# Optimization experiments

Hardware: AMD Instinct MI355X
Metric: run time of the kernel (lower is better)

The kernel has to match this reference:

```python
import jax, jax.numpy as jnp
import numpy as np
from jax import lax

EPS = 1e-5
B, CIN, H, W = 4, 512, 64, 64
CI = CIN // 4          # inter_channels = 128
CQK = CI // 8          # PAM query/key channels = 16
NC = 19                # num_classes


def conv2d(x, w, pad):
    return lax.conv_general_dilated(x, w, (1, 1), [(pad, pad), (pad, pad)],
                                    dimension_numbers=('NCHW', 'OIHW', 'NCHW'))


def bn_relu(x, g, b, m, v):
    # eval-mode BatchNorm2d followed by ReLU
    inv = g * lax.rsqrt(v + EPS)
    return jax.nn.relu(x * inv[None, :, None, None] + (b - m * inv)[None, :, None, None])


def setup_inputs() -> dict:
    key = jax.random.key(0)
    ks = iter(jax.random.split(key, 40))
    rn = lambda shape, s=0.02: (jax.random.normal(next(ks), shape, dtype=jnp.float32) * s)
    ones = lambda n: jnp.ones((n,), jnp.float32)
    zeros = lambda n: jnp.zeros((n,), jnp.float32)
    inp = {
        'x': jax.random.normal(next(ks), (B, CIN, H, W), dtype=jnp.float32),
        # conv_p1: 3x3 conv (no bias) + BN
        'wp1': rn((CI, CIN, 3, 3)),
        'bnp1_w': ones(CI), 'bnp1_b': zeros(CI), 'bnp1_m': zeros(CI), 'bnp1_v': ones(CI),
        # PAM 1x1 convs
        'qw': rn((CQK, CI, 1, 1)), 'qb': zeros(CQK),
        'kw': rn((CQK, CI, 1, 1)), 'kb': zeros(CQK),
        'vw': rn((CI, CI, 1, 1)), 'vb': zeros(CI),
        'pam_gamma': jnp.full((1,), 0.5, jnp.float32),
        # conv_p2
        'wp2': rn((CI, CI, 3, 3)),
        'bnp2_w': ones(CI), 'bnp2_b': zeros(CI), 'bnp2_m': zeros(CI), 'bnp2_v': ones(CI),
        # conv_c1
        'wc1': rn((CI, CIN, 3, 3)),
        'bnc1_w': ones(CI), 'bnc1_b': zeros(CI), 'bnc1_m': zeros(CI), 'bnc1_v': ones(CI),
        'cam_gamma': jnp.full((1,), 0.5, jnp.float32),
        # conv_c2
        'wc2': rn((CI, CI, 3, 3)),
        'bnc2_w': ones(CI), 'bnc2_b': zeros(CI), 'bnc2_m': zeros(CI), 'bnc2_v': ones(CI),
        # classifier heads (dropout is eval-mode identity)
        'cls_w': rn((NC, CI, 1, 1)), 'cls_b': zeros(NC),
        'auxp_w': rn((NC, CI, 1, 1)), 'auxp_b': zeros(NC),
        'auxc_w': rn((NC, CI, 1, 1)), 'auxc_b': zeros(NC),
    }
    return inp


def pam(x, qw, qb, kw, kb, vw, vb, gamma):
    b, c, h, w = x.shape
    n = h * w
    q = (conv2d(x, qw, 0) + qb[None, :, None, None]).reshape(b, -1, n)  # [B,CQK,N]
    k = (conv2d(x, kw, 0) + kb[None, :, None, None]).reshape(b, -1, n)  # [B,CQK,N]
    v = (conv2d(x, vw, 0) + vb[None, :, None, None]).reshape(b, c, n)   # [B,C,N]
    attn = jax.nn.softmax(jnp.einsum('bcn,bcm->bnm', q, k), axis=-1)    # [B,N,N]
    out = jnp.einsum('bcm,bnm->bcn', v, attn).reshape(b, c, h, w)
    return gamma * out + x


def cam(x, gamma):
    b, c, h, w = x.shape
    f = x.reshape(b, c, -1)                                             # [B,C,N]
    attn = jax.nn.softmax(jnp.einsum('bin,bjn->bij', f, f), axis=-1)    # [B,C,C]
    out = jnp.einsum('bij,bjn->bin', attn, f).reshape(b, c, h, w)
    return gamma * out + x


def _forward(x, wp1, bnp1_w, bnp1_b, bnp1_m, bnp1_v,
             qw, qb, kw, kb, vw, vb, pam_gamma,
             wp2, bnp2_w, bnp2_b, bnp2_m, bnp2_v,
             wc1, bnc1_w, bnc1_b, bnc1_m, bnc1_v, cam_gamma,
             wc2, bnc2_w, bnc2_b, bnc2_m, bnc2_v,
             cls_w, cls_b, auxp_w, auxp_b, auxc_w, auxc_b):
    feat_p = bn_relu(conv2d(x, wp1, 1), bnp1_w, bnp1_b, bnp1_m, bnp1_v)
    feat_p = pam(feat_p, qw, qb, kw, kb, vw, vb, pam_gamma)
    feat_p = bn_relu(conv2d(feat_p, wp2, 1), bnp2_w, bnp2_b, bnp2_m, bnp2_v)

    feat_c = bn_relu(conv2d(x, wc1, 1), bnc1_w, bnc1_b, bnc1_m, bnc1_v)
    feat_c = cam(feat_c, cam_gamma)
    feat_c = bn_relu(conv2d(feat_c, wc2, 1), bnc2_w, bnc2_b, bnc2_m, bnc2_v)

    feat = feat_p + feat_c
    out = conv2d(feat, cls_w, 0) + cls_b[None, :, None, None]
    out_p = conv2d(feat_p, auxp_w, 0) + auxp_b[None, :, None, None]
    out_c = conv2d(feat_c, auxc_w, 0) + auxc_b[None, :, None, None]
    return out, out_p, out_c


def reference(x, wp1, bnp1_w, bnp1_b, bnp1_m, bnp1_v,
              qw, qb, kw, kb, vw, vb, pam_gamma,
              wp2, bnp2_w, bnp2_b, bnp2_m, bnp2_v,
              wc1, bnc1_w, bnc1_b, bnc1_m, bnc1_v, cam_gamma,
              wc2, bnc2_w, bnc2_b, bnc2_m, bnc2_v,
              cls_w, cls_b, auxp_w, auxp_b, auxc_w, auxc_b):
    return _forward(x, wp1, bnp1_w, bnp1_b, bnp1_m, bnp1_v,
                    qw, qb, kw, kb, vw, vb, pam_gamma,
                    wp2, bnp2_w, bnp2_b, bnp2_m, bnp2_v,
                    wc1, bnc1_w, bnc1_b, bnc1_m, bnc1_v, cam_gamma,
                    wc2, bnc2_w, bnc2_b, bnc2_m, bnc2_v,
                    cls_w, cls_b, auxp_w, auxp_b, auxc_w, auxc_b)
```

## Files before the change

### kernel.cpp

```cpp
#include <hip/hip_runtime.h>
#include <cstdint>
#include <cstddef>


using s16x8 = __attribute__((ext_vector_type(8))) short;
using u16x8 = __attribute__((ext_vector_type(8))) unsigned short;
using u16x4 = __attribute__((ext_vector_type(4))) unsigned short;
using f32x4 = __attribute__((ext_vector_type(4))) float;
using f32x16 = __attribute__((ext_vector_type(16))) float;
using u32x4v = __attribute__((ext_vector_type(4))) unsigned;

__device__ __forceinline__ f32x4 mfma16(u16x8 a, u16x8 b, f32x4 c) {
  return __builtin_amdgcn_mfma_f32_16x16x32_bf16(
      __builtin_bit_cast(s16x8, a), __builtin_bit_cast(s16x8, b), c, 0, 0, 0);
}
__device__ __forceinline__ f32x16 mfma32(u16x8 a, u16x8 b, f32x16 c) {
  return __builtin_amdgcn_mfma_f32_32x32x16_bf16(
      __builtin_bit_cast(s16x8, a), __builtin_bit_cast(s16x8, b), c, 0, 0, 0);
}
__device__ __forceinline__ float bf2f(unsigned short u) {
  return __builtin_bit_cast(float, (unsigned)u << 16);
}
__device__ __forceinline__ unsigned short f2bf(float f) {
  unsigned u = __builtin_bit_cast(unsigned, f);
  u += 0x7fffu + ((u >> 16) & 1u);
  return (unsigned short)(u >> 16);
}
__device__ __forceinline__ unsigned cvt_pk_bf16(float lo, float hi) {
  unsigned r;
  asm("v_cvt_pk_bf16_f32 %0, %1, %2" : "=v"(r) : "v"(lo), "v"(hi));
  return r;
}
__device__ __forceinline__ u16x8 ld8(const unsigned short* p) {
  return *reinterpret_cast<const u16x8*>(p);
}
__device__ __forceinline__ void gload16(const void* g, void* l) {
  __builtin_amdgcn_global_load_lds(
      (const __attribute__((address_space(1))) void*)g,
      (__attribute__((address_space(3))) void*)l, 16, 0, 0);
}

#define OFF_XT    ((size_t)0)
#define OFF_FP1   ((size_t)19464192)
#define OFF_FC1   ((size_t)24330240)
#define ZERO_BYTES ((size_t)29196288)
#define OFF_FP0   ((size_t)29196288)
#define OFF_FC0   ((size_t)33390592)
#define OFF_FP2   ((size_t)37584896)
#define OFF_FC2   ((size_t)41779200)
#define OFF_WT1   ((size_t)45973504)
#define OFF_WT2   ((size_t)48332800)
#define OFF_QKW   ((size_t)48922624)
#define OFF_VWW   ((size_t)48930816)
#define OFF_HWW   ((size_t)48963584)
#define OFF_BNSS  ((size_t)48988160)
#define OFF_ATTN  ((size_t)48992256)
#define OFF_Q     OFF_FP2
#define OFF_K     (OFF_FP2 + 524288)
#define OFF_V     OFF_FC2

__global__ __launch_bounds__(256) void k_xpose(const float* __restrict__ x,
                                               unsigned short* __restrict__ xt) {
  __shared__ float tile[128][65];
  const int t = threadIdx.x;
  const int blk = blockIdx.x;
  const int cb = blk & 3;
  const int h = (blk >> 2) & 63;
  const int b = blk >> 8;
  const float* src = x + ((size_t)(b * 512 + cb * 128) * 64 + h) * 64;
  const int w = t & 63, cr = t >> 6;
  for (int i = 0; i < 32; ++i) tile[cr + i * 4][w] = src[(size_t)(cr + i * 4) * 4096 + w];
  __syncthreads();
  const int w2 = t >> 2, cg = t & 3;
  const int cic = cb * 2 + (cg >> 1);
  const int kk = ((w2 + 1) & 7) << 3;
  unsigned short* dst =
      xt + (((size_t)(b * 8 + cic) * 66 + h + 1) * 72 + (w2 + 1)) * 64 + (cg & 1) * 32;
#pragma unroll
  for (int j = 0; j < 32; j += 4) {
    const int sb = (cg >> 1) * 64 + (((cg & 1) * 32 + j) ^ kk);
    u16x4 pk;
    pk[0] = f2bf(tile[sb + 0][w2]);
    pk[1] = f2bf(tile[sb + 1][w2]);
    pk[2] = f2bf(tile[sb + 2][w2]);
    pk[3] = f2bf(tile[sb + 3][w2]);
    *reinterpret_cast<u16x4*>(dst + j) = pk;
  }
}

struct PackArgs {
  const float *wp1, *wc1, *wp2, *wc2, *qw, *kw, *vw, *clsw, *apw, *acw;
  const float *g1p, *b1p, *m1p, *v1p, *g1c, *b1c, *m1c, *v1c;
  const float *g2p, *b2p, *m2p, *v2p, *g2c, *b2c, *m2c, *v2c;
  unsigned short *wt1, *wt2, *qkw, *vww, *hww;
  float* bnss;
};
__global__ __launch_bounds__(256) void k_pack(PackArgs A) {
  const int i = blockIdx.x * 256 + threadIdx.x;
  const int N1 = 2 * 8 * 9 * 128 * 64;
  const int N2 = N1 + 2 * 2 * 9 * 128 * 64;
  const int N3 = N2 + 2 * 16 * 128;
  const int N4 = N3 + 128 * 128;
  const int N5 = N4 + 3 * 32 * 128;
  const int N6 = N5 + 8 * 128;
  if (i < N1) {
    int ci = i & 63, co = (i >> 6) & 127;
    int rest = i >> 13;
    int tap = rest % 9, cc = rest / 9;
    int cic = cc & 7, brr = cc >> 3;
    const float* s = brr ? A.wc1 : A.wp1;
    int cis = ci ^ ((co & 7) << 3);
    A.wt1[i] = f2bf(s[(size_t)(co * 512 + cic * 64 + cis) * 9 + tap]);
  } else if (i < N2) {
    int k = i - N1;
    int ci = k & 63, co = (k >> 6) & 127;
    int rest = k >> 13;
    int tap = rest % 9, cc = rest / 9;
    int cic = cc & 1, brr = cc >> 1;
    const float* s = brr ? A.wc2 : A.wp2;
    int cis = ci ^ ((co & 7) << 3);
    A.wt2[k] = f2bf(s[(size_t)(co * 128 + cic * 64 + cis) * 9 + tap]);
  } else if (i < N3) {
    int k = i - N2;
    int ci = k & 127, q = k >> 7;
    const float* s = (q < 16) ? A.qw : A.kw;
    A.qkw[k] = f2bf(s[(q & 15) * 128 + ci]);
  } else if (i < N4) {
    int k = i - N3;
    A.vww[k] = f2bf(A.vw[k]);
  } else if (i < N5) {
    int k = i - N4;
    int ci = k & 127, co = (k >> 7) & 31, hd = k >> 12;
    const float* s = hd == 0 ? A.clsw : (hd == 1 ? A.apw : A.acw);
    A.hww[k] = (co < 19) ? f2bf(s[co * 128 + ci]) : (unsigned short)0;
  } else if (i < N6) {
    int k = i - N5;
    int j = k & 127, seg = k >> 7;
    const float *g, *bb, *mm, *vv;
    switch (seg >> 1) {
      case 0: g = A.g1p; bb = A.b1p; mm = A.m1p; vv = A.v1p; break;
      case 1: g = A.g1c; bb = A.b1c; mm = A.m1c; vv = A.v1c; break;
      case 2: g = A.g2p; bb = A.b2p; mm = A.m2p; vv = A.v2p; break;
      default: g = A.g2c; bb = A.b2c; mm = A.m2c; vv = A.v2c; break;
    }
    float sc = g[j] * rsqrtf(vv[j] + 1e-5f);
    A.bnss[k] = (seg & 1) ? (bb[j] - mm[j] * sc) : sc;
  }
}

template <int NCHUNK>
__global__ __launch_bounds__(256, 1) void k_conv3x3(
    const unsigned short* __restrict__ in0, const unsigned short* __restrict__ in1,
    const unsigned short* __restrict__ wt, const float* __restrict__ bnb,
    unsigned short* __restrict__ out0, unsigned short* __restrict__ out1) {
  __shared__ unsigned short Awin[4 * 72 * 64];
  __shared__ unsigned short Wbuf[2][3 * 128 * 64];
  const int bid = blockIdx.x;
  const int ht = bid & 31;
  const int b = (bid >> 5) & 3;
  const int br = bid >> 7;
  const unsigned short* inp = br ? in1 : in0;
  const unsigned short* wbr = wt + (size_t)br * NCHUNK * 9 * 128 * 64;
  const float* scale = bnb + br * 256;
  const float* shiftp = scale + 128;
  unsigned short* outp = br ? out1 : out0;
  const int tid = threadIdx.x;
  const int lane = tid & 63, wv = tid >> 6;
  const int l31 = lane & 31, hi = lane >> 5;
  const int hi16 = hi * 16;
  const int nq = wv & 1, ch = wv >> 1;
  const int wn = nq * 64, cob = ch * 64;
  const int h0 = ht * 2;

  int aw[2], arow[2];
#pragma unroll
  for (int mf = 0; mf < 2; ++mf) {
    int n = wn + mf * 32 + l31;
    aw[mf] = n & 63;
    arow[mf] = (n >> 6) * 72;
  }
  int bvbase[2];
#pragma unroll
  for (int nf = 0; nf < 2; ++nf) bvbase[nf] = (cob + nf * 32 + l31) * 128;
  const int bkey = (l31 & 7) << 4;

  f32x16 acc[2][2];
#pragma unroll
  for (int mf = 0; mf < 2; ++mf)
#pragma unroll
    for (int nf = 0; nf < 2; ++nf) acc[mf][nf] = (f32x16)0.f;

  u16x8 streg[9];
  auto sloadA = [&](int c) {
    const char* sr =
        (const char*)(inp + (((size_t)(b * NCHUNK + c) * 66 + h0) * 72) * 64);
#pragma unroll
    for (int i = 0; i < 9; ++i)
      streg[i] = *(const u16x8*)(sr + i * 4096 + tid * 16);
  };
  auto swriteA = [&]() {
    char* dp = (char*)Awin;
#pragma unroll
    for (int i = 0; i < 9; ++i)
      *(u16x8*)(dp + i * 4096 + tid * 16) = streg[i];
  };
  auto stageW = [&](int bi, int T) {
    const char* src = (const char*)wbr + (size_t)T * 49152;
    char* dst = (char*)&Wbuf[bi][0];
#pragma unroll
    for (int i = 0; i < 12; ++i)
      gload16(src + i * 4096 + tid * 16, dst + i * 4096 + tid * 16);
  };

  auto compute = [&](int g, int bi) {
    const char* ab = (const char*)Awin;
    const char* wb = (const char*)&Wbuf[bi][0];
#pragma unroll
    for (int tl = 0; tl < 3; ++tl) {
      int abase[2], akey[2];
#pragma unroll
      for (int mf = 0; mf < 2; ++mf) {
        int wc = aw[mf] + tl;
        abase[mf] = ((arow[mf] + g * 72 + wc) << 7);
        akey[mf] = (wc & 7) << 4;
      }
      const int wtl = tl << 14;
#pragma unroll
      for (int s = 0; s < 4; ++s) {
        const int ko = s * 32 + hi16;
        u16x8 av[2], bv[2];
#pragma unroll
        for (int mf = 0; mf < 2; ++mf)
          av[mf] = *(const u16x8*)(ab + abase[mf] + (ko ^ akey[mf]));
#pragma unroll
        for (int nf = 0; nf < 2; ++nf)
          bv[nf] = *(const u16x8*)(wb + wtl + bvbase[nf] + (ko ^ bkey));
#pragma unroll
        for (int mf = 0; mf < 2; ++mf)
#pragma unroll
          for (int nf = 0; nf < 2; ++nf)
            acc[mf][nf] = mfma32(av[mf], bv[nf], acc[mf][nf]);
      }
    }
  };

  const int total = 3 * NCHUNK;
  sloadA(0);
  stageW(0, 0);
  swriteA();
  stageW(1, 1);
  asm volatile("s_waitcnt vmcnt(12) lgkmcnt(0)\ns_barrier" ::: "memory");
  if (NCHUNK > 1) sloadA(1);

#pragma unroll 1
  for (int c = 0; c < NCHUNK; ++c) {
#pragma unroll
    for (int g = 0; g < 3; ++g) {
      const int T = c * 3 + g;
      compute(g, T & 1);
      if (T + 1 < total) {
        asm volatile("s_waitcnt lgkmcnt(0)\ns_barrier" ::: "memory");
        bool issuedA = false;
        if (g == 2) {
          swriteA();
          if (c + 2 < NCHUNK) {
            sloadA(c + 2);
            issuedA = true;
          }
        }
        if (T + 2 < total) {
          stageW((T + 2) & 1, T + 2);
          if (issuedA)
            asm volatile("s_waitcnt vmcnt(21) lgkmcnt(0)\ns_barrier" ::: "memory");
          else
            asm volatile("s_waitcnt vmcnt(12) lgkmcnt(0)\ns_barrier" ::: "memory");
        } else {
          asm volatile("s_waitcnt vmcnt(0) lgkmcnt(0)\ns_barrier" ::: "memory");
        }
      }
    }
  }

#pragma unroll
  for (int nf = 0; nf < 2; ++nf) {
    const int co = cob + nf * 32 + l31;
    const float sc = scale[co], sh = shiftp[co];
#pragma unroll
    for (int mf = 0; mf < 2; ++mf)
#pragma unroll
      for (int r = 0; r < 16; ++r) {
        int n = wn + mf * 32 + (r & 3) + 8 * (r >> 2) + 4 * hi;
        float y = acc[mf][nf][r] * sc + sh;
        y = y > 0.f ? y : 0.f;
        outp[((size_t)b * 4096 + (size_t)(h0 + (n >> 6)) * 64 + (n & 63)) * 128 + co] =
            f2bf(y);
      }
  }
}

__global__ __launch_bounds__(256) void k_qkv(
    const unsigned short* __restrict__ fp0, const unsigned short* __restrict__ qkw,
    const unsigned short* __restrict__ vww, const float* __restrict__ qb,
    const float* __restrict__ kb, const float* __restrict__ vb,
    unsigned short* __restrict__ Q, unsigned short* __restrict__ K,
    unsigned short* __restrict__ V2) {
  const int bid = blockIdx.x;
  const int nt = bid & 63, b = bid >> 6;
  const int lane = threadIdx.x & 63, wv = threadIdx.x >> 6;
  const int lg = lane >> 4, l15 = lane & 15;
  const int n = nt * 64 + wv * 16 + l15;
  const unsigned short* fbase = fp0 + ((size_t)b * 4096 + n) * 128 + lg * 8;
  f32x4 vacc[8];
#pragma unroll
  for (int mf = 0; mf < 8; ++mf) vacc[mf] = (f32x4){0.f, 0.f, 0.f, 0.f};
  f32x4 qacc = {0.f, 0.f, 0.f, 0.f}, kacc = {0.f, 0.f, 0.f, 0.f};
#pragma unroll
  for (int kc = 0; kc < 128; kc += 32) {
    u16x8 fb = ld8(fbase + kc);
    u16x8 qa = ld8(qkw + (size_t)l15 * 128 + lg * 8 + kc);
    u16x8 ka = ld8(qkw + 2048 + (size_t)l15 * 128 + lg * 8 + kc);
    qacc = mfma16(qa, fb, qacc);
    kacc = mfma16(ka, fb, kacc);
#pragma unroll
    for (int mf = 0; mf < 8; ++mf) {
      u16x8 va = ld8(vww + (size_t)(mf * 16 + l15) * 128 + lg * 8 + kc);
      vacc[mf] = mfma16(va, fb, vacc[mf]);
    }
  }
  const float LOG2E = 1.44269504088896f;
#pragma unroll
  for (int r = 0; r < 4; ++r) {
    int cq = lg * 4 + r;
    Q[(size_t)(b * 4096 + n) * 16 + cq] = f2bf((qacc[r] + qb[cq]) * LOG2E);
    K[(size_t)(b * 4096 + n) * 16 + cq] = f2bf(kacc[r] + kb[cq]);
  }
#pragma unroll
  for (int mf = 0; mf < 8; ++mf)
#pragma unroll
    for (int r = 0; r < 4; ++r) {
      int c = mf * 16 + lg * 4 + r;
      V2[((size_t)(b * 512 + (n >> 3)) * 128 + c) * 8 + (n & 7)] =
          f2bf(vacc[mf][r] + vb[c]);
    }
}

__global__ __launch_bounds__(512, 1) void k_pam(
    const unsigned short* __restrict__ Q, const unsigned short* __restrict__ K,
    const unsigned short* __restrict__ V2, const unsigned short* __restrict__ fp0,
    unsigned short* __restrict__ fp1, const float* __restrict__ pg) {
  __shared__ float obuf[2][3][16][64][4];
  __shared__ float lred[8][64];
  const int bid = blockIdx.x;
  const int qt = bid & 63, b = bid >> 6;
  const int tid = threadIdx.x;
  const int lane = tid & 63, wv = tid >> 6;
  const int qsub = wv >> 2, mq = wv & 3;
  const int l31 = lane & 31, hi = lane >> 5;
  const int q0 = qt * 64 + qsub * 32;
  const unsigned short* Qp = Q + (size_t)b * 65536;
  const unsigned short* Kp = K + (size_t)b * 65536;
  const unsigned short* Vp = V2 + (size_t)b * 524288;
  const int hi8 = hi * 8;

  const u16x8 qB = ld8(Qp + (size_t)(q0 + l31) * 16 + hi8);

  f32x16 oacc[4];
#pragma unroll
  for (int ch = 0; ch < 4; ++ch) oacc[ch] = (f32x16)0.f;
  float dsum = 0.f;

  auto loadK = [&](int t) -> u16x8 {
    return ld8(Kp + (size_t)(t * 32 + l31) * 16 + hi8);
  };
  auto loadV = [&](int t, u16x8 (&vf)[8]) {
#pragma unroll
    for (int kc = 0; kc < 2; ++kc)
#pragma unroll
      for (int ch = 0; ch < 4; ++ch)
        vf[kc * 4 + ch] =
            ld8(Vp + (size_t)(t * 4 + kc * 2 + hi) * 1024 + (ch * 32 + l31) * 8);
  };
  auto body = [&](u16x8 kA, u16x8 (&vf)[8]) {
    f32x16 pacc = mfma32(kA, qB, (f32x16)0.f);
    float p[16];
#pragma unroll
    for (int r = 0; r < 16; ++r) p[r] = exp2f(pacc[r]);
    dsum += (((p[0] + p[1]) + (p[2] + p[3])) + ((p[4] + p[5]) + (p[6] + p[7]))) +
            (((p[8] + p[9]) + (p[10] + p[11])) + ((p[12] + p[13]) + (p[14] + p[15])));
    unsigned X[8], S[8];
#pragma unroll
    for (int j = 0; j < 8; ++j) X[j] = cvt_pk_bf16(p[2 * j], p[2 * j + 1]);
#pragma unroll
    for (int j = 0; j < 8; ++j) S[j] = __shfl_xor(X[j], 32, 64);
    const bool hc = hi != 0;
    u32x4v w0, w1;
    w0[0] = hc ? S[2] : X[0];
    w0[1] = hc ? S[3] : X[1];
    w0[2] = hc ? X[2] : S[0];
    w0[3] = hc ? X[3] : S[1];
    w1[0] = hc ? S[6] : X[4];
    w1[1] = hc ? S[7] : X[5];
    w1[2] = hc ? X[6] : S[4];
    w1[3] = hc ? X[7] : S[5];
    u16x8 f0 = __builtin_bit_cast(u16x8, w0);
    u16x8 f1 = __builtin_bit_cast(u16x8, w1);
#pragma unroll
    for (int ch = 0; ch < 4; ++ch) oacc[ch] = mfma32(f0, vf[ch], oacc[ch]);
#pragma unroll
    for (int ch = 0; ch < 4; ++ch) oacc[ch] = mfma32(f1, vf[4 + ch], oacc[ch]);
  };

  const int t0 = mq * 32;
  u16x8 kA0 = loadK(t0), kA1;
  u16x8 vf0[8], vf1[8];
  loadV(t0, vf0);
#pragma unroll 1
  for (int t = 0; t < 32; t += 2) {
    kA1 = loadK(t0 + t + 1);
    loadV(t0 + t + 1, vf1);
    body(kA0, vf0);
    if (t + 2 < 32) {
      kA0 = loadK(t0 + t + 2);
      loadV(t0 + t + 2, vf0);
    }
    body(kA1, vf1);
  }

  dsum += __shfl_xor(dsum, 32, 64);
  lred[wv][lane] = dsum;
  if (mq) {
#pragma unroll
    for (int ch = 0; ch < 4; ++ch)
#pragma unroll
      for (int j = 0; j < 4; ++j) {
        f32x4 v = {oacc[ch][4 * j + 0], oacc[ch][4 * j + 1], oacc[ch][4 * j + 2],
                   oacc[ch][4 * j + 3]};
        *reinterpret_cast<f32x4*>(&obuf[qsub][mq - 1][ch * 4 + j][lane][0]) = v;
      }
  }
  __syncthreads();
  if (mq == 0) {
    const float dtot = lred[qsub * 4 + 0][lane] + lred[qsub * 4 + 1][lane] +
                       lred[qsub * 4 + 2][lane] + lred[qsub * 4 + 3][lane];
#pragma unroll
    for (int ch = 0; ch < 4; ++ch)
#pragma unroll
      for (int j = 0; j < 4; ++j) {
        f32x4 s0 = *reinterpret_cast<const f32x4*>(&obuf[qsub][0][ch * 4 + j][lane][0]);
        f32x4 s1 = *reinterpret_cast<const f32x4*>(&obuf[qsub][1][ch * 4 + j][lane][0]);
        f32x4 s2 = *reinterpret_cast<const f32x4*>(&obuf[qsub][2][ch * 4 + j][lane][0]);
#pragma unroll
        for (int r = 0; r < 4; ++r)
          oacc[ch][4 * j + r] += (s0[r] + s1[r]) + s2[r];
      }
    const float rden = 1.f / dtot;
    const float gm = pg[0];
    float rdr[16];
#pragma unroll
    for (int r = 0; r < 16; ++r)
      rdr[r] = __shfl(rden, (r & 3) + 8 * (r >> 2) + 4 * hi, 64);
#pragma unroll
    for (int ch = 0; ch < 4; ++ch) {
      const int c = ch * 32 + l31;
#pragma unroll
      for (int r = 0; r < 16; ++r) {
        const int n = q0 + (r & 3) + 8 * (r >> 2) + 4 * hi;
        const int wp = (n & 63) + 1;
        float o = gm * oacc[ch][r] * rdr[r] +
                  bf2f(fp0[((size_t)b * 4096 + n) * 128 + c]);
        fp1[(((size_t)(b * 2 + (c >> 6)) * 66 + (n >> 6) + 1) * 72 + wp) * 64 +
            ((c & 63) ^ ((wp & 7) << 3))] = f2bf(o);
      }
    }
  }
}

__global__ __launch_bounds__(256) void k_gram(const unsigned short* __restrict__ fc0,
                                              float* __restrict__ Gp) {
  __shared__ float fl[32][132];
  const int bid = blockIdx.x;
  const int nc = bid & 63, b = bid >> 6;
  const int t = threadIdx.x;
  const int i = t >> 1, jh = (t & 1) * 64;
  float acc[64];
#pragma unroll
  for (int j = 0; j < 64; ++j) acc[j] = 0.f;
  for (int c2 = 0; c2 < 2; ++c2) {
    const int n0 = nc * 64 + c2 * 32;
    {
      int nn = t >> 3, kh = t & 7;
      const unsigned short* src = fc0 + ((size_t)b * 4096 + n0 + nn) * 128 + kh * 16;
      u16x8 v0 = ld8(src), v1 = ld8(src + 8);
#pragma unroll
      for (int e = 0; e < 8; ++e) {
        fl[nn][kh * 16 + e] = bf2f(v0[e]);
        fl[nn][kh * 16 + 8 + e] = bf2f(v1[e]);
      }
    }
    __syncthreads();
    for (int nn = 0; nn < 32; ++nn) {
      float fi = fl[nn][i];
      const float4* row = reinterpret_cast<const float4*>(&fl[nn][jh]);
#pragma unroll
      for (int j4 = 0; j4 < 16; ++j4) {
        float4 fv = row[j4];
        acc[4 * j4 + 0] += fi * fv.x;
        acc[4 * j4 + 1] += fi * fv.y;
        acc[4 * j4 + 2] += fi * fv.z;
        acc[4 * j4 + 3] += fi * fv.w;
      }
    }
    __syncthreads();
  }
  float* dst = Gp + (((size_t)b * 64 + nc) * 128 + i) * 128 + jh;
  float4* dst4 = reinterpret_cast<float4*>(dst);
#pragma unroll
  for (int j4 = 0; j4 < 16; ++j4)
    dst4[j4] = make_float4(acc[4 * j4], acc[4 * j4 + 1], acc[4 * j4 + 2], acc[4 * j4 + 3]);
}

__global__ __launch_bounds__(128) void k_softm(const float* __restrict__ Gp,
                                               unsigned short* __restrict__ attn) {
  const int bid = blockIdx.x;
  const int i = bid & 127, b = bid >> 7;
  const int j = threadIdx.x;
  float g = 0.f;
  for (int nc = 0; nc < 64; ++nc) g += Gp[(((size_t)b * 64 + nc) * 128 + i) * 128 + j];
  __shared__ float red[2], red2[2];
  float m = g;
  m = fmaxf(m, __shfl_xor(m, 1, 64));
  m = fmaxf(m, __shfl_xor(m, 2, 64));
  m = fmaxf(m, __shfl_xor(m, 4, 64));
  m = fmaxf(m, __shfl_xor(m, 8, 64));
  m = fmaxf(m, __shfl_xor(m, 16, 64));
  m = fmaxf(m, __shfl_xor(m, 32, 64));
  const int wvi = j >> 6;
  if ((j & 63) == 0) red[wvi] = m;
  __syncthreads();
  m = fmaxf(red[0], red[1]);
  float e = __expf(g - m);
  float s = e;
  s += __shfl_xor(s, 1, 64);
  s += __shfl_xor(s, 2, 64);
  s += __shfl_xor(s, 4, 64);
  s += __shfl_xor(s, 8, 64);
  s += __shfl_xor(s, 16, 64);
  s += __shfl_xor(s, 32, 64);
  if ((j & 63) == 0) red2[wvi] = s;
  __syncthreads();
  s = red2[0] + red2[1];
  attn[((size_t)b * 128 + i) * 128 + j] = f2bf(e / s);
}

__global__ __launch_bounds__(256) void k_camout(
    const unsigned short* __restrict__ fc0, const unsigned short* __restrict__ attn,
    const float* __restrict__ cg, unsigned short* __restrict__ fc1) {
  const int bid = blockIdx.x;
  const int nt = bid & 63, b = bid >> 6;
  const int lane = threadIdx.x & 63, wv = threadIdx.x >> 6;
  const int lg = lane >> 4, l15 = lane & 15;
  const int n = nt * 64 + wv * 16 + l15;
  const unsigned short* fbase = fc0 + ((size_t)b * 4096 + n) * 128 + lg * 8;
  const unsigned short* abase = attn + (size_t)b * 16384 + lg * 8;
  f32x4 acc[8];
#pragma unroll
  for (int mf = 0; mf < 8; ++mf) acc[mf] = (f32x4){0.f, 0.f, 0.f, 0.f};
#pragma unroll
  for (int kc = 0; kc < 128; kc += 32) {
    u16x8 fb = ld8(fbase + kc);
#pragma unroll
    for (int mf = 0; mf < 8; ++mf) {
      u16x8 aa = ld8(abase + (size_t)(mf * 16 + l15) * 128 + kc);
      acc[mf] = mfma16(aa, fb, acc[mf]);
    }
  }
  const float gm = cg[0];
  const int nn = nt * 64 + wv * 16 + l15;
  const int wp = (nn & 63) + 1;
#pragma unroll
  for (int mf = 0; mf < 8; ++mf)
#pragma unroll
    for (int r = 0; r < 4; ++r) {
      int c = mf * 16 + lg * 4 + r;
      float o = gm * acc[mf][r] + bf2f(fc0[((size_t)b * 4096 + nn) * 128 + c]);
      fc1[(((size_t)(b * 2 + (c >> 6)) * 66 + (nn >> 6) + 1) * 72 + wp) * 64 +
          ((c & 63) ^ ((wp & 7) << 3))] = f2bf(o);
    }
}

__global__ __launch_bounds__(256) void k_heads(
    const unsigned short* __restrict__ fp2, const unsigned short* __restrict__ fc2,
    const unsigned short* __restrict__ hw, const float* __restrict__ clsb,
    const float* __restrict__ apb, const float* __restrict__ acb,
    float* __restrict__ out) {
  const int bid = blockIdx.x;
  const int nt = bid & 63, b = bid >> 6;
  const int lane = threadIdx.x & 63, wv = threadIdx.x >> 6;
  const int lg = lane >> 4, l15 = lane & 15;
  const int n = nt * 64 + wv * 16 + l15;
  const unsigned short* pb = fp2 + (size_t)(b * 4096 + n) * 128 + lg * 8;
  const unsigned short* cb = fc2 + (size_t)(b * 4096 + n) * 128 + lg * 8;
  f32x4 acc[3][2];
#pragma unroll
  for (int hd = 0; hd < 3; ++hd)
#pragma unroll
    for (int mf = 0; mf < 2; ++mf) acc[hd][mf] = (f32x4){0.f, 0.f, 0.f, 0.f};
#pragma unroll
  for (int kc = 0; kc < 128; kc += 32) {
    u16x8 vp = ld8(pb + kc);
    u16x8 vc = ld8(cb + kc);
    u16x8 vs;
#pragma unroll
    for (int e = 0; e < 8; ++e) vs[e] = f2bf(bf2f(vp[e]) + bf2f(vc[e]));
#pragma unroll
    for (int mf = 0; mf < 2; ++mf) {
      u16x8 a0 = ld8(hw + (size_t)(0 * 32 + mf * 16 + l15) * 128 + lg * 8 + kc);
      u16x8 a1 = ld8(hw + (size_t)(1 * 32 + mf * 16 + l15) * 128 + lg * 8 + kc);
      u16x8 a2 = ld8(hw + (size_t)(2 * 32 + mf * 16 + l15) * 128 + lg * 8 + kc);
      acc[0][mf] = mfma16(a0, vs, acc[0][mf]);
      acc[1][mf] = mfma16(a1, vp, acc[1][mf]);
      acc[2][mf] = mfma16(a2, vc, acc[2][mf]);
    }
  }
  const float* bias[3] = {clsb, apb, acb};
  const size_t hoff[3] = {0, 311296, 622592};
#pragma unroll
  for (int hd = 0; hd < 3; ++hd)
#pragma unroll
    for (int mf = 0; mf < 2; ++mf)
#pragma unroll
      for (int r = 0; r < 4; ++r) {
        int co = mf * 16 + lg * 4 + r;
        if (co < 19)
          out[hoff[hd] + ((size_t)b * 19 + co) * 4096 + n] = acc[hd][mf][r] + bias[hd][co];
      }
}

extern "C" void kernel_launch(void* const* d_in, const int* in_sizes, int n_in,
                              void* d_out, int out_size, void* d_ws, size_t ws_size,
                              hipStream_t stream) {
  (void)in_sizes; (void)n_in; (void)out_size; (void)ws_size;
  const float* x = (const float*)d_in[0];
  const float* wp1 = (const float*)d_in[1];
  const float* g1p = (const float*)d_in[2];
  const float* b1p = (const float*)d_in[3];
  const float* m1p = (const float*)d_in[4];
  const float* v1p = (const float*)d_in[5];
  const float* qw = (const float*)d_in[6];
  const float* qb = (const float*)d_in[7];
  const float* kw = (const float*)d_in[8];
  const float* kb = (const float*)d_in[9];
  const float* vw = (const float*)d_in[10];
  const float* vb = (const float*)d_in[11];
  const float* pamg = (const float*)d_in[12];
  const float* wp2 = (const float*)d_in[13];
  const float* g2p = (const float*)d_in[14];
  const float* b2p = (const float*)d_in[15];
  const float* m2p = (const float*)d_in[16];
  const float* v2p = (const float*)d_in[17];
  const float* wc1 = (const float*)d_in[18];
  const float* g1c = (const float*)d_in[19];
  const float* b1c = (const float*)d_in[20];
  const float* m1c = (const float*)d_in[21];
  const float* v1c = (const float*)d_in[22];
  const float* camg = (const float*)d_in[23];
  const float* wc2 = (const float*)d_in[24];
  const float* g2c = (const float*)d_in[25];
  const float* b2c = (const float*)d_in[26];
  const float* m2c = (const float*)d_in[27];
  const float* v2c = (const float*)d_in[28];
  const float* clsw = (const float*)d_in[29];
  const float* clsb = (const float*)d_in[30];
  const float* apw = (const float*)d_in[31];
  const float* apb = (const float*)d_in[32];
  const float* acw = (const float*)d_in[33];
  const float* acb = (const float*)d_in[34];

  char* ws = (char*)d_ws;
  unsigned short* xt = (unsigned short*)(ws + OFF_XT);
  unsigned short* fp1 = (unsigned short*)(ws + OFF_FP1);
  unsigned short* fc1 = (unsigned short*)(ws + OFF_FC1);
  unsigned short* fp0 = (unsigned short*)(ws + OFF_FP0);
  unsigned short* fc0 = (unsigned short*)(ws + OFF_FC0);
  unsigned short* fp2 = (unsigned short*)(ws + OFF_FP2);
  unsigned short* fc2 = (unsigned short*)(ws + OFF_FC2);
  unsigned short* wt1 = (unsigned short*)(ws + OFF_WT1);
  unsigned short* wt2 = (unsigned short*)(ws + OFF_WT2);
  unsigned short* qkw = (unsigned short*)(ws + OFF_QKW);
  unsigned short* vww = (unsigned short*)(ws + OFF_VWW);
  unsigned short* hww = (unsigned short*)(ws + OFF_HWW);
  float* bnss = (float*)(ws + OFF_BNSS);
  unsigned short* Qb = (unsigned short*)(ws + OFF_Q);
  unsigned short* Kb = (unsigned short*)(ws + OFF_K);
  unsigned short* Vb = (unsigned short*)(ws + OFF_V);
  unsigned short* attnb = (unsigned short*)(ws + OFF_ATTN);
  float* Gp = (float*)(ws + OFF_XT);

  hipMemsetAsync(ws, 0, ZERO_BYTES, stream);

  PackArgs pa;
  pa.wp1 = wp1; pa.wc1 = wc1; pa.wp2 = wp2; pa.wc2 = wc2;
  pa.qw = qw; pa.kw = kw; pa.vw = vw; pa.clsw = clsw; pa.apw = apw; pa.acw = acw;
  pa.g1p = g1p; pa.b1p = b1p; pa.m1p = m1p; pa.v1p = v1p;
  pa.g1c = g1c; pa.b1c = b1c; pa.m1c = m1c; pa.v1c = v1c;
  pa.g2p = g2p; pa.b2p = b2p; pa.m2p = m2p; pa.v2p = v2p;
  pa.g2c = g2c; pa.b2c = b2c; pa.m2c = m2c; pa.v2c = v2c;
  pa.wt1 = wt1; pa.wt2 = wt2; pa.qkw = qkw; pa.vww = vww; pa.hww = hww; pa.bnss = bnss;
  k_pack<<<5892, 256, 0, stream>>>(pa);

  k_xpose<<<1024, 256, 0, stream>>>(x, xt);

  k_conv3x3<8><<<256, 256, 0, stream>>>(xt, xt, wt1, bnss, fp0, fc0);

  k_qkv<<<256, 256, 0, stream>>>(fp0, qkw, vww, qb, kb, vb, Qb, Kb, Vb);
  k_gram<<<256, 256, 0, stream>>>(fc0, Gp);
  k_pam<<<256, 512, 0, stream>>>(Qb, Kb, Vb, fp0, fp1, pamg);
  k_softm<<<512, 128, 0, stream>>>(Gp, attnb);
  k_camout<<<256, 256, 0, stream>>>(fc0, attnb, camg, fc1);

  k_conv3x3<2><<<256, 256, 0, stream>>>(fp1, fc1, wt2, bnss + 512, fp2, fc2);

  k_heads<<<256, 256, 0, stream>>>(fp2, fc2, hww, clsb, apb, acb, (float*)d_out);
}
```

Before: 197.2 us.

## Split conv3x3 output channels across blocks with per-tap weight staging

```diff
diff --git a/kernel.cpp b/kernel.cpp
--- a/kernel.cpp
+++ b/kernel.cpp
@@ -73,17 +73,15 @@
   __syncthreads();
   const int w2 = t >> 2, cg = t & 3;
   const int cic = cb * 2 + (cg >> 1);
-  const int kk = ((w2 + 1) & 7) << 3;
   unsigned short* dst =
       xt + (((size_t)(b * 8 + cic) * 66 + h + 1) * 72 + (w2 + 1)) * 64 + (cg & 1) * 32;
 #pragma unroll
   for (int j = 0; j < 32; j += 4) {
-    const int sb = (cg >> 1) * 64 + (((cg & 1) * 32 + j) ^ kk);
     u16x4 pk;
-    pk[0] = f2bf(tile[sb + 0][w2]);
-    pk[1] = f2bf(tile[sb + 1][w2]);
-    pk[2] = f2bf(tile[sb + 2][w2]);
-    pk[3] = f2bf(tile[sb + 3][w2]);
+    pk[0] = f2bf(tile[cg * 32 + j + 0][w2]);
+    pk[1] = f2bf(tile[cg * 32 + j + 1][w2]);
+    pk[2] = f2bf(tile[cg * 32 + j + 2][w2]);
+    pk[3] = f2bf(tile[cg * 32 + j + 3][w2]);
     *reinterpret_cast<u16x4*>(dst + j) = pk;
   }
 }
@@ -97,28 +95,30 @@
 };
 __global__ __launch_bounds__(256) void k_pack(PackArgs A) {
   const int i = blockIdx.x * 256 + threadIdx.x;
-  const int N1 = 2 * 8 * 9 * 128 * 64;
-  const int N2 = N1 + 2 * 2 * 9 * 128 * 64;
+  const int N1 = 2 * 2 * 8 * 9 * 64 * 64;
+  const int N2 = N1 + 2 * 2 * 2 * 9 * 64 * 64;
   const int N3 = N2 + 2 * 16 * 128;
   const int N4 = N3 + 128 * 128;
   const int N5 = N4 + 3 * 32 * 128;
   const int N6 = N5 + 8 * 128;
   if (i < N1) {
-    int ci = i & 63, co = (i >> 6) & 127;
-    int rest = i >> 13;
-    int tap = rest % 9, cc = rest / 9;
-    int cic = cc & 7, brr = cc >> 3;
+    int ci = i & 63, co64 = (i >> 6) & 63;
+    int rest = i >> 12;
+    int tap = rest % 9, rest2 = rest / 9;
+    int cic = rest2 & 7, chh = (rest2 >> 3) & 1, brr = rest2 >> 4;
     const float* s = brr ? A.wc1 : A.wp1;
-    int cis = ci ^ ((co & 7) << 3);
+    int co = chh * 64 + co64;
+    int cis = ci ^ (((co ^ (co >> 3)) & 7) << 3);
     A.wt1[i] = f2bf(s[(size_t)(co * 512 + cic * 64 + cis) * 9 + tap]);
   } else if (i < N2) {
     int k = i - N1;
-    int ci = k & 63, co = (k >> 6) & 127;
-    int rest = k >> 13;
-    int tap = rest % 9, cc = rest / 9;
-    int cic = cc & 1, brr = cc >> 1;
+    int ci = k & 63, co64 = (k >> 6) & 63;
+    int rest = k >> 12;
+    int tap = rest % 9, rest2 = rest / 9;
+    int cic = rest2 & 1, chh = (rest2 >> 1) & 1, brr = rest2 >> 2;
     const float* s = brr ? A.wc2 : A.wp2;
-    int cis = ci ^ ((co & 7) << 3);
+    int co = chh * 64 + co64;
+    int cis = ci ^ (((co ^ (co >> 3)) & 7) << 3);
     A.wt2[k] = f2bf(s[(size_t)(co * 128 + cic * 64 + cis) * 9 + tap]);
   } else if (i < N3) {
     int k = i - N2;
@@ -149,18 +149,19 @@
 }
 
 template <int NCHUNK>
-__global__ __launch_bounds__(256, 1) void k_conv3x3(
+__global__ __launch_bounds__(256, 2) void k_conv3x3(
     const unsigned short* __restrict__ in0, const unsigned short* __restrict__ in1,
     const unsigned short* __restrict__ wt, const float* __restrict__ bnb,
     unsigned short* __restrict__ out0, unsigned short* __restrict__ out1) {
   __shared__ unsigned short Awin[4 * 72 * 64];
-  __shared__ unsigned short Wbuf[2][3 * 128 * 64];
+  __shared__ unsigned short Wbuf[2][64 * 64];
   const int bid = blockIdx.x;
-  const int ht = bid & 31;
-  const int b = (bid >> 5) & 3;
-  const int br = bid >> 7;
+  const int ch = bid & 1;
+  const int ht = (bid >> 1) & 31;
+  const int b = (bid >> 6) & 3;
+  const int br = bid >> 8;
   const unsigned short* inp = br ? in1 : in0;
-  const unsigned short* wbr = wt + (size_t)br * NCHUNK * 9 * 128 * 64;
+  const unsigned short* wbr = wt + (size_t)(br * 2 + ch) * NCHUNK * 9 * 64 * 64;
   const float* scale = bnb + br * 256;
   const float* shiftp = scale + 128;
   unsigned short* outp = br ? out1 : out0;
@@ -168,27 +169,15 @@
   const int lane = tid & 63, wv = tid >> 6;
   const int l31 = lane & 31, hi = lane >> 5;
   const int hi16 = hi * 16;
-  const int nq = wv & 1, ch = wv >> 1;
-  const int wn = nq * 64, cob = ch * 64;
   const int h0 = ht * 2;
-
-  int aw[2], arow[2];
-#pragma unroll
-  for (int mf = 0; mf < 2; ++mf) {
-    int n = wn + mf * 32 + l31;
-    aw[mf] = n & 63;
-    arow[mf] = (n >> 6) * 72;
-  }
-  int bvbase[2];
-#pragma unroll
-  for (int nf = 0; nf < 2; ++nf) bvbase[nf] = (cob + nf * 32 + l31) * 128;
-  const int bkey = (l31 & 7) << 4;
-
-  f32x16 acc[2][2];
-#pragma unroll
-  for (int mf = 0; mf < 2; ++mf)
-#pragma unroll
-    for (int nf = 0; nf < 2; ++nf) acc[mf][nf] = (f32x16)0.f;
+  const int cog = ch * 64;
+
+  const int n = wv * 32 + l31;
+  const int oh = n >> 6, w = n & 63;
+
+  f32x16 acc[2];
+  acc[0] = (f32x16)0.f;
+  acc[1] = (f32x16)0.f;
 
   u16x8 streg[9];
   auto sloadA = [&](int c) {
@@ -201,81 +190,63 @@
   auto swriteA = [&]() {
     char* dp = (char*)Awin;
 #pragma unroll
-    for (int i = 0; i < 9; ++i)
-      *(u16x8*)(dp + i * 4096 + tid * 16) = streg[i];
+    for (int i = 0; i < 9; ++i) {
+      int g = i * 32 + (tid >> 3);
+      int row = g / 72;
+      int col = g - row * 72;
+      int key = ((col ^ (col >> 3)) & 7) << 4;
+      *(u16x8*)(dp + g * 128 + (((tid & 7) * 16) ^ key)) = streg[i];
+    }
   };
   auto stageW = [&](int bi, int T) {
-    const char* src = (const char*)wbr + (size_t)T * 49152;
+    const char* src = (const char*)wbr + (size_t)T * 8192;
     char* dst = (char*)&Wbuf[bi][0];
 #pragma unroll
-    for (int i = 0; i < 12; ++i)
-      gload16(src + i * 4096 + tid * 16, dst + i * 4096 + tid * 16);
+    for (int i = 0; i < 2; ++i)
+      gload16(src + (wv * 2 + i) * 1024 + lane * 16, dst + (wv * 2 + i) * 1024);
   };
-
-  auto compute = [&](int g, int bi) {
+  auto compute_tap = [&](int ty, int tx, int bi) {
     const char* ab = (const char*)Awin;
     const char* wb = (const char*)&Wbuf[bi][0];
-#pragma unroll
-    for (int tl = 0; tl < 3; ++tl) {
-      int abase[2], akey[2];
-#pragma unroll
-      for (int mf = 0; mf < 2; ++mf) {
-        int wc = aw[mf] + tl;
-        abase[mf] = ((arow[mf] + g * 72 + wc) << 7);
-        akey[mf] = (wc & 7) << 4;
-      }
-      const int wtl = tl << 14;
-#pragma unroll
-      for (int s = 0; s < 4; ++s) {
-        const int ko = s * 32 + hi16;
-        u16x8 av[2], bv[2];
-#pragma unroll
-        for (int mf = 0; mf < 2; ++mf)
-          av[mf] = *(const u16x8*)(ab + abase[mf] + (ko ^ akey[mf]));
-#pragma unroll
-        for (int nf = 0; nf < 2; ++nf)
-          bv[nf] = *(const u16x8*)(wb + wtl + bvbase[nf] + (ko ^ bkey));
-#pragma unroll
-        for (int mf = 0; mf < 2; ++mf)
-#pragma unroll
-          for (int nf = 0; nf < 2; ++nf)
-            acc[mf][nf] = mfma32(av[mf], bv[nf], acc[mf][nf]);
-      }
+    const int wc = w + tx;
+    const int abase = ((oh + ty) * 72 + wc) << 7;
+    const int akey = ((wc ^ (wc >> 3)) & 7) << 4;
+    const int c0 = l31, c1 = 32 + l31;
+    const int b0 = c0 * 128, k0 = ((c0 ^ (c0 >> 3)) & 7) << 4;
+    const int b1 = c1 * 128, k1 = ((c1 ^ (c1 >> 3)) & 7) << 4;
+#pragma unroll
+    for (int s = 0; s < 4; ++s) {
+      const int ko = s * 32 + hi16;
+      u16x8 av = *(const u16x8*)(ab + abase + (ko ^ akey));
+      u16x8 bv0 = *(const u16x8*)(wb + b0 + (ko ^ k0));
+      u16x8 bv1 = *(const u16x8*)(wb + b1 + (ko ^ k1));
+      acc[0] = mfma32(av, bv0, acc[0]);
+      acc[1] = mfma32(av, bv1, acc[1]);
     }
   };
 
-  const int total = 3 * NCHUNK;
   sloadA(0);
+  swriteA();
   stageW(0, 0);
-  swriteA();
-  stageW(1, 1);
-  asm volatile("s_waitcnt vmcnt(12) lgkmcnt(0)\ns_barrier" ::: "memory");
-  if (NCHUNK > 1) sloadA(1);
+  asm volatile("s_waitcnt vmcnt(0) lgkmcnt(0)\ns_barrier" ::: "memory");
 
 #pragma unroll 1
   for (int c = 0; c < NCHUNK; ++c) {
 #pragma unroll
-    for (int g = 0; g < 3; ++g) {
-      const int T = c * 3 + g;
-      compute(g, T & 1);
-      if (T + 1 < total) {
-        asm volatile("s_waitcnt lgkmcnt(0)\ns_barrier" ::: "memory");
-        bool issuedA = false;
-        if (g == 2) {
+    for (int t = 0; t < 9; ++t) {
+      const int T = c * 9 + t;
+      if (T + 1 < NCHUNK * 9) stageW((T + 1) & 1, T + 1);
+      const bool ldA = (t == 3 && c + 1 < NCHUNK);
+      if (ldA) sloadA(c + 1);
+      compute_tap(t / 3, t % 3, T & 1);
+      if (T + 1 < NCHUNK * 9) {
+        if (ldA)
+          asm volatile("s_waitcnt vmcnt(9) lgkmcnt(0)\ns_barrier" ::: "memory");
+        else
+          asm volatile("s_waitcnt vmcnt(0) lgkmcnt(0)\ns_barrier" ::: "memory");
+        if (t == 8) {
           swriteA();
-          if (c + 2 < NCHUNK) {
-            sloadA(c + 2);
-            issuedA = true;
-          }
-        }
-        if (T + 2 < total) {
-          stageW((T + 2) & 1, T + 2);
-          if (issuedA)
-            asm volatile("s_waitcnt vmcnt(21) lgkmcnt(0)\ns_barrier" ::: "memory");
-          else
-            asm volatile("s_waitcnt vmcnt(12) lgkmcnt(0)\ns_barrier" ::: "memory");
-        } else {
-          asm volatile("s_waitcnt vmcnt(0) lgkmcnt(0)\ns_barrier" ::: "memory");
+          asm volatile("s_waitcnt lgkmcnt(0)\ns_barrier" ::: "memory");
         }
       }
     }
@@ -283,18 +254,16 @@
 
 #pragma unroll
   for (int nf = 0; nf < 2; ++nf) {
-    const int co = cob + nf * 32 + l31;
+    const int co = cog + nf * 32 + l31;
     const float sc = scale[co], sh = shiftp[co];
 #pragma unroll
-    for (int mf = 0; mf < 2; ++mf)
-#pragma unroll
-      for (int r = 0; r < 16; ++r) {
-        int n = wn + mf * 32 + (r & 3) + 8 * (r >> 2) + 4 * hi;
-        float y = acc[mf][nf][r] * sc + sh;
-        y = y > 0.f ? y : 0.f;
-        outp[((size_t)b * 4096 + (size_t)(h0 + (n >> 6)) * 64 + (n & 63)) * 128 + co] =
-            f2bf(y);
-      }
+    for (int r = 0; r < 16; ++r) {
+      int nr = wv * 32 + (r & 3) + 8 * (r >> 2) + 4 * hi;
+      float y = acc[nf][r] * sc + sh;
+      y = y > 0.f ? y : 0.f;
+      outp[((size_t)b * 4096 + (size_t)(h0 + (nr >> 6)) * 64 + (nr & 63)) * 128 + co] =
+          f2bf(y);
+    }
   }
 }
 
@@ -465,11 +434,11 @@
 #pragma unroll
       for (int r = 0; r < 16; ++r) {
         const int n = q0 + (r & 3) + 8 * (r >> 2) + 4 * hi;
-        const int wp = (n & 63) + 1;
         float o = gm * oacc[ch][r] * rdr[r] +
                   bf2f(fp0[((size_t)b * 4096 + n) * 128 + c]);
-        fp1[(((size_t)(b * 2 + (c >> 6)) * 66 + (n >> 6) + 1) * 72 + wp) * 64 +
-            ((c & 63) ^ ((wp & 7) << 3))] = f2bf(o);
+        fp1[(((size_t)(b * 2 + (c >> 6)) * 66 + (n >> 6) + 1) * 72 + ((n & 63) + 1)) *
+                64 +
+            (c & 63)] = f2bf(o);
       }
     }
   }
@@ -576,15 +545,14 @@
   }
   const float gm = cg[0];
   const int nn = nt * 64 + wv * 16 + l15;
-  const int wp = (nn & 63) + 1;
 #pragma unroll
   for (int mf = 0; mf < 8; ++mf)
 #pragma unroll
     for (int r = 0; r < 4; ++r) {
       int c = mf * 16 + lg * 4 + r;
       float o = gm * acc[mf][r] + bf2f(fc0[((size_t)b * 4096 + nn) * 128 + c]);
-      fc1[(((size_t)(b * 2 + (c >> 6)) * 66 + (nn >> 6) + 1) * 72 + wp) * 64 +
-          ((c & 63) ^ ((wp & 7) << 3))] = f2bf(o);
+      fc1[(((size_t)(b * 2 + (c >> 6)) * 66 + (nn >> 6) + 1) * 72 + (nn & 63) + 1) * 64 +
+          (c & 63)] = f2bf(o);
     }
 }
 
@@ -710,7 +678,7 @@
 
   k_xpose<<<1024, 256, 0, stream>>>(x, xt);
 
-  k_conv3x3<8><<<256, 256, 0, stream>>>(xt, xt, wt1, bnss, fp0, fc0);
+  k_conv3x3<8><<<512, 256, 0, stream>>>(xt, xt, wt1, bnss, fp0, fc0);
 
   k_qkv<<<256, 256, 0, stream>>>(fp0, qkw, vww, qb, kb, vb, Qb, Kb, Vb);
   k_gram<<<256, 256, 0, stream>>>(fc0, Gp);
@@ -718,7 +686,7 @@
   k_softm<<<512, 128, 0, stream>>>(Gp, attnb);
   k_camout<<<256, 256, 0, stream>>>(fc0, attnb, camg, fc1);
 
-  k_conv3x3<2><<<256, 256, 0, stream>>>(fp1, fc1, wt2, bnss + 512, fp2, fc2);
+  k_conv3x3<2><<<512, 256, 0, stream>>>(fp1, fc1, wt2, bnss + 512, fp2, fc2);
 
   k_heads<<<256, 256, 0, stream>>>(fp2, fc2, hww, clsb, apb, acb, (float*)d_out);
 }
```

After: 206.5 us. 4.7% more time.

## Restage conv3x3 weights per tap with triple buffering and on-write LDS swizzle

Applied to the files above, without the earlier changes.

```diff
diff --git a/kernel.cpp b/kernel.cpp
--- a/kernel.cpp
+++ b/kernel.cpp
@@ -73,17 +73,15 @@
   __syncthreads();
   const int w2 = t >> 2, cg = t & 3;
   const int cic = cb * 2 + (cg >> 1);
-  const int kk = ((w2 + 1) & 7) << 3;
   unsigned short* dst =
       xt + (((size_t)(b * 8 + cic) * 66 + h + 1) * 72 + (w2 + 1)) * 64 + (cg & 1) * 32;
 #pragma unroll
   for (int j = 0; j < 32; j += 4) {
-    const int sb = (cg >> 1) * 64 + (((cg & 1) * 32 + j) ^ kk);
     u16x4 pk;
-    pk[0] = f2bf(tile[sb + 0][w2]);
-    pk[1] = f2bf(tile[sb + 1][w2]);
-    pk[2] = f2bf(tile[sb + 2][w2]);
-    pk[3] = f2bf(tile[sb + 3][w2]);
+    pk[0] = f2bf(tile[cg * 32 + j + 0][w2]);
+    pk[1] = f2bf(tile[cg * 32 + j + 1][w2]);
+    pk[2] = f2bf(tile[cg * 32 + j + 2][w2]);
+    pk[3] = f2bf(tile[cg * 32 + j + 3][w2]);
     *reinterpret_cast<u16x4*>(dst + j) = pk;
   }
 }
@@ -109,7 +107,7 @@
     int tap = rest % 9, cc = rest / 9;
     int cic = cc & 7, brr = cc >> 3;
     const float* s = brr ? A.wc1 : A.wp1;
-    int cis = ci ^ ((co & 7) << 3);
+    int cis = ci ^ (((co ^ (co >> 3)) & 7) << 3);
     A.wt1[i] = f2bf(s[(size_t)(co * 512 + cic * 64 + cis) * 9 + tap]);
   } else if (i < N2) {
     int k = i - N1;
@@ -118,7 +116,7 @@
     int tap = rest % 9, cc = rest / 9;
     int cic = cc & 1, brr = cc >> 1;
     const float* s = brr ? A.wc2 : A.wp2;
-    int cis = ci ^ ((co & 7) << 3);
+    int cis = ci ^ (((co ^ (co >> 3)) & 7) << 3);
     A.wt2[k] = f2bf(s[(size_t)(co * 128 + cic * 64 + cis) * 9 + tap]);
   } else if (i < N3) {
     int k = i - N2;
@@ -154,7 +152,7 @@
     const unsigned short* __restrict__ wt, const float* __restrict__ bnb,
     unsigned short* __restrict__ out0, unsigned short* __restrict__ out1) {
   __shared__ unsigned short Awin[4 * 72 * 64];
-  __shared__ unsigned short Wbuf[2][3 * 128 * 64];
+  __shared__ unsigned short Wbuf[3][128 * 64];
   const int bid = blockIdx.x;
   const int ht = bid & 31;
   const int b = (bid >> 5) & 3;
@@ -168,21 +166,23 @@
   const int lane = tid & 63, wv = tid >> 6;
   const int l31 = lane & 31, hi = lane >> 5;
   const int hi16 = hi * 16;
-  const int nq = wv & 1, ch = wv >> 1;
-  const int wn = nq * 64, cob = ch * 64;
+  const int wn = (wv & 1) * 64, cob = (wv >> 1) * 64;
   const int h0 = ht * 2;
 
-  int aw[2], arow[2];
+  int agrp[2], aw[2];
 #pragma unroll
   for (int mf = 0; mf < 2; ++mf) {
     int n = wn + mf * 32 + l31;
     aw[mf] = n & 63;
-    arow[mf] = (n >> 6) * 72;
-  }
-  int bvbase[2];
-#pragma unroll
-  for (int nf = 0; nf < 2; ++nf) bvbase[nf] = (cob + nf * 32 + l31) * 128;
-  const int bkey = (l31 & 7) << 4;
+    agrp[mf] = (n >> 6) * 72;
+  }
+  int bbase[2], bkey[2];
+#pragma unroll
+  for (int nf = 0; nf < 2; ++nf) {
+    int co = cob + nf * 32 + l31;
+    bbase[nf] = co * 128;
+    bkey[nf] = ((co ^ (co >> 3)) & 7) << 4;
+  }
 
   f32x16 acc[2][2];
 #pragma unroll
@@ -201,82 +201,82 @@
   auto swriteA = [&]() {
     char* dp = (char*)Awin;
 #pragma unroll
-    for (int i = 0; i < 9; ++i)
-      *(u16x8*)(dp + i * 4096 + tid * 16) = streg[i];
+    for (int i = 0; i < 9; ++i) {
+      int g = i * 32 + (tid >> 3);
+      int row = g / 72;
+      int col = g - row * 72;
+      int key = ((col ^ (col >> 3)) & 7) << 4;
+      *(u16x8*)(dp + g * 128 + (((tid & 7) * 16) ^ key)) = streg[i];
+    }
   };
   auto stageW = [&](int bi, int T) {
-    const char* src = (const char*)wbr + (size_t)T * 49152;
+    const char* src = (const char*)wbr + (size_t)T * 16384;
     char* dst = (char*)&Wbuf[bi][0];
 #pragma unroll
-    for (int i = 0; i < 12; ++i)
+    for (int i = 0; i < 4; ++i)
       gload16(src + i * 4096 + tid * 16, dst + i * 4096 + tid * 16);
   };
-
-  auto compute = [&](int g, int bi) {
+  auto compute_tap = [&](int ty, int tx, int bi) {
     const char* ab = (const char*)Awin;
     const char* wb = (const char*)&Wbuf[bi][0];
-#pragma unroll
-    for (int tl = 0; tl < 3; ++tl) {
-      int abase[2], akey[2];
-#pragma unroll
-      for (int mf = 0; mf < 2; ++mf) {
-        int wc = aw[mf] + tl;
-        abase[mf] = ((arow[mf] + g * 72 + wc) << 7);
-        akey[mf] = (wc & 7) << 4;
-      }
-      const int wtl = tl << 14;
-#pragma unroll
-      for (int s = 0; s < 4; ++s) {
-        const int ko = s * 32 + hi16;
-        u16x8 av[2], bv[2];
-#pragma unroll
-        for (int mf = 0; mf < 2; ++mf)
-          av[mf] = *(const u16x8*)(ab + abase[mf] + (ko ^ akey[mf]));
+    int abase[2], akey[2];
+#pragma unroll
+    for (int mf = 0; mf < 2; ++mf) {
+      int wc = aw[mf] + tx;
+      abase[mf] = (agrp[mf] + ty * 72 + wc) << 7;
+      akey[mf] = ((wc ^ (wc >> 3)) & 7) << 4;
+    }
+#pragma unroll
+    for (int s = 0; s < 4; ++s) {
+      const int ko = s * 32 + hi16;
+      u16x8 av[2], bv[2];
+#pragma unroll
+      for (int mf = 0; mf < 2; ++mf)
+        av[mf] = *(const u16x8*)(ab + abase[mf] + (ko ^ akey[mf]));
+#pragma unroll
+      for (int nf = 0; nf < 2; ++nf)
+        bv[nf] = *(const u16x8*)(wb + bbase[nf] + (ko ^ bkey[nf]));
+#pragma unroll
+      for (int mf = 0; mf < 2; ++mf)
 #pragma unroll
         for (int nf = 0; nf < 2; ++nf)
-          bv[nf] = *(const u16x8*)(wb + wtl + bvbase[nf] + (ko ^ bkey));
-#pragma unroll
-        for (int mf = 0; mf < 2; ++mf)
-#pragma unroll
-          for (int nf = 0; nf < 2; ++nf)
-            acc[mf][nf] = mfma32(av[mf], bv[nf], acc[mf][nf]);
-      }
+          acc[mf][nf] = mfma32(av[mf], bv[nf], acc[mf][nf]);
     }
   };
 
-  const int total = 3 * NCHUNK;
+  const int total = 9 * NCHUNK;
   sloadA(0);
+  swriteA();
   stageW(0, 0);
-  swriteA();
   stageW(1, 1);
-  asm volatile("s_waitcnt vmcnt(12) lgkmcnt(0)\ns_barrier" ::: "memory");
-  if (NCHUNK > 1) sloadA(1);
+  asm volatile("s_waitcnt vmcnt(4) lgkmcnt(0)" ::: "memory");
+  __builtin_amdgcn_s_barrier();
 
 #pragma unroll 1
   for (int c = 0; c < NCHUNK; ++c) {
-#pragma unroll
-    for (int g = 0; g < 3; ++g) {
-      const int T = c * 3 + g;
-      compute(g, T & 1);
-      if (T + 1 < total) {
-        asm volatile("s_waitcnt lgkmcnt(0)\ns_barrier" ::: "memory");
-        bool issuedA = false;
-        if (g == 2) {
-          swriteA();
-          if (c + 2 < NCHUNK) {
-            sloadA(c + 2);
-            issuedA = true;
-          }
-        }
-        if (T + 2 < total) {
-          stageW((T + 2) & 1, T + 2);
-          if (issuedA)
-            asm volatile("s_waitcnt vmcnt(21) lgkmcnt(0)\ns_barrier" ::: "memory");
-          else
-            asm volatile("s_waitcnt vmcnt(12) lgkmcnt(0)\ns_barrier" ::: "memory");
-        } else {
-          asm volatile("s_waitcnt vmcnt(0) lgkmcnt(0)\ns_barrier" ::: "memory");
-        }
+    const bool pf = (c + 1 < NCHUNK);
+#pragma unroll
+    for (int t = 0; t < 9; ++t) {
+      const int T = c * 9 + t;
+      if (T + 2 < total) stageW((T + 2) % 3, T + 2);
+      if (t == 0 && pf) sloadA(c + 1);
+      compute_tap(t / 3, t - (t / 3) * 3, T % 3);
+      if (T + 1 == total) break;
+      if (t == 8) {
+        asm volatile("s_waitcnt lgkmcnt(0)" ::: "memory");
+        __builtin_amdgcn_s_barrier();
+        swriteA();
+        asm volatile("s_waitcnt vmcnt(4) lgkmcnt(0)" ::: "memory");
+        __builtin_amdgcn_s_barrier();
+      } else if (pf && t < 2) {
+        asm volatile("s_waitcnt vmcnt(13) lgkmcnt(0)" ::: "memory");
+        __builtin_amdgcn_s_barrier();
+      } else if (T + 2 < total) {
+        asm volatile("s_waitcnt vmcnt(4) lgkmcnt(0)" ::: "memory");
+        __builtin_amdgcn_s_barrier();
+      } else {
+        asm volatile("s_waitcnt vmcnt(0) lgkmcnt(0)" ::: "memory");
+        __builtin_amdgcn_s_barrier();
       }
     }
   }
@@ -465,11 +465,11 @@
 #pragma unroll
       for (int r = 0; r < 16; ++r) {
         const int n = q0 + (r & 3) + 8 * (r >> 2) + 4 * hi;
-        const int wp = (n & 63) + 1;
         float o = gm * oacc[ch][r] * rdr[r] +
                   bf2f(fp0[((size_t)b * 4096 + n) * 128 + c]);
-        fp1[(((size_t)(b * 2 + (c >> 6)) * 66 + (n >> 6) + 1) * 72 + wp) * 64 +
-            ((c & 63) ^ ((wp & 7) << 3))] = f2bf(o);
+        fp1[(((size_t)(b * 2 + (c >> 6)) * 66 + (n >> 6) + 1) * 72 + ((n & 63) + 1)) *
+                64 +
+            (c & 63)] = f2bf(o);
       }
     }
   }
@@ -576,15 +576,14 @@
   }
   const float gm = cg[0];
   const int nn = nt * 64 + wv * 16 + l15;
-  const int wp = (nn & 63) + 1;
 #pragma unroll
   for (int mf = 0; mf < 8; ++mf)
 #pragma unroll
     for (int r = 0; r < 4; ++r) {
       int c = mf * 16 + lg * 4 + r;
       float o = gm * acc[mf][r] + bf2f(fc0[((size_t)b * 4096 + nn) * 128 + c]);
-      fc1[(((size_t)(b * 2 + (c >> 6)) * 66 + (nn >> 6) + 1) * 72 + wp) * 64 +
-          ((c & 63) ^ ((wp & 7) << 3))] = f2bf(o);
+      fc1[(((size_t)(b * 2 + (c >> 6)) * 66 + (nn >> 6) + 1) * 72 + (nn & 63) + 1) * 64 +
+          (c & 63)] = f2bf(o);
     }
 }
 
```

Result: no change. 198.4 us (+0.6%).
